# Optimization experiments

Hardware: AMD Instinct MI355X
Metric: run time of the kernel (lower is better)

Reference implementation:

```python
import jax, jax.numpy as jnp
import numpy as np
from jax import lax

N, CIN, COUT = 4, 3, 16
D = H = W = 64
K, S, PAD, OUT_PAD = 3, 2, 1, 1


def setup_inputs() -> dict:
    key = jax.random.key(0)
    k1, k2, k3, k4 = jax.random.split(key, 4)
    x = jax.random.normal(k1, (N, CIN, D, H, W), dtype=jnp.float32)
    # torch ConvTranspose3d weight layout: [Cin, Cout, kD, kH, kW]
    w = jax.random.normal(k2, (CIN, COUT, K, K, K), dtype=jnp.float32) * 0.1
    b = jax.random.normal(k3, (COUT,), dtype=jnp.float32) * 0.1
    subtract = jax.random.normal(k4, (COUT,), dtype=jnp.float32) * 0.1
    return {"x": x, "w": w, "b": b, "subtract": subtract}


def reference(x, w, b, subtract):
    # ConvTranspose3d(k=3, s=2, p=1, output_padding=1) as a dilated conv:
    # flip kernel spatially, swap in/out channel axes, lhs_dilation = stride,
    # padding low = k-1-p = 1, padding high = k-1-p+output_padding = 2.
    w_conv = jnp.flip(jnp.transpose(w, (1, 0, 2, 3, 4)), axis=(2, 3, 4))  # [Cout,Cin,k,k,k]
    y = lax.conv_general_dilated(
        x, w_conv,
        window_strides=(1, 1, 1),
        padding=[(1, 2), (1, 2), (1, 2)],
        lhs_dilation=(S, S, S),
        dimension_numbers=("NCDHW", "OIDHW", "NCDHW"),
    )  # [N, 16, 2D, 2H, 2W]
    y = y + b[None, :, None, None, None]
    # MaxPool3d(kernel=2, stride=2, pad=0)
    y = lax.reduce_window(
        y, -jnp.inf, lax.max,
        window_dimensions=(1, 1, 2, 2, 2),
        window_strides=(1, 1, 2, 2, 2),
        padding="VALID",
    )  # [N, 16, D, H, W]
    s = jax.nn.softmax(y, axis=1)                       # channel softmax
    z = s - subtract[None, :, None, None, None]          # per-channel subtract
    sw = z * jax.nn.sigmoid(z)                           # swish
    return jnp.max(sw, axis=1)                           # max over channels -> [N, D, H, W]
```

## Files before the change

### kernel.cpp

```cpp
#include <hip/hip_runtime.h>
#include <math.h>

#define CIN 3
#define COUT 16
#define DHW 64


typedef float f8 __attribute__((ext_vector_type(8)));
typedef float f2 __attribute__((ext_vector_type(2)));

struct WBuf { f8 a, b, c; f2 d2; float dl; };

template <int G>
static __device__ __forceinline__ void wload(WBuf& b, const float* wbase) {
    constexpr int CO = G / 3, C = G % 3;
    constexpr int BOFF = (C * COUT + CO) * 27 * 4;
    asm volatile(
        "s_load_dwordx8 %0, %5, %6\n\t"
        "s_load_dwordx8 %1, %5, %7\n\t"
        "s_load_dwordx8 %2, %5, %8\n\t"
        "s_load_dwordx2 %3, %5, %9\n\t"
        "s_load_dword   %4, %5, %10"
        : "=s"(b.a), "=s"(b.b), "=s"(b.c), "=s"(b.d2), "=s"(b.dl)
        : "s"(wbase), "i"(BOFF), "i"(BOFF + 32), "i"(BOFF + 64),
          "i"(BOFF + 96), "i"(BOFF + 104));
}

static __device__ __forceinline__ void wwait(WBuf& b) {
    asm volatile("s_waitcnt lgkmcnt(0)"
                 : "+s"(b.a), "+s"(b.b), "+s"(b.c), "+s"(b.d2), "+s"(b.dl));
}

static __device__ __forceinline__ float welem(const WBuf& w, int k) {
    return k < 8 ? w.a[k] : k < 16 ? w.b[k - 8] : k < 24 ? w.c[k - 16]
                 : k < 26 ? w.d2[k - 24] : w.dl;
}

template <int C>
static __device__ __forceinline__ void fma_group(
    const WBuf& wb, const float (&xr)[CIN][3][2][3], float (&acc)[8][4]) {
#pragma unroll
    for (int kd = 0; kd < 3; ++kd) {
        const int pd  = (kd == 1) ? 0 : 1;
        const int dlt = (kd == 0) ? 1 : 0;
#pragma unroll
        for (int kh = 0; kh < 3; ++kh) {
            const int ph = (kh == 1) ? 0 : 1;
            const int hh = (kh == 0) ? 1 : 0;
#pragma unroll
            for (int kw = 0; kw < 3; ++kw) {
                const int pw = (kw == 1) ? 0 : 1;
                const int ww = (kw == 0) ? 1 : 0;
                const float wt = welem(wb, kd * 9 + kh * 3 + kw);
                const int q = (pd * 2 + ph) * 2 + pw;
#pragma unroll
                for (int dout = 0; dout < 2; ++dout)
#pragma unroll
                    for (int vx = 0; vx < 2; ++vx) {
                        const float xv = xr[C][dout + dlt][hh][ww + vx];
                        const int v = dout * 2 + vx;
                        if (C == 0 && kd < 2 && kh < 2 && kw < 2)
                            acc[q][v] = wt * xv;
                        else
                            acc[q][v] = fmaf(wt, xv, acc[q][v]);
                    }
            }
        }
    }
}

static __device__ __forceinline__ void pool_close(const float (&acc)[8][4],
                                                  float (&pc)[4]) {
#pragma unroll
    for (int v = 0; v < 4; ++v) {
        const float m01 = fmaxf(acc[0][v], acc[1][v]);
        const float m23 = fmaxf(acc[2][v], acc[3][v]);
        const float m45 = fmaxf(acc[4][v], acc[5][v]);
        const float m67 = fmaxf(acc[6][v], acc[7][v]);
        pc[v] = fmaxf(fmaxf(m01, m23), fmaxf(m45, m67));
    }
}

template <int G>
struct Pipe {
    static __device__ __forceinline__ void run(
        WBuf& A, WBuf& B, const float* w, const float (&xr)[CIN][3][2][3],
        float (&acc)[8][4], float (&pooled)[COUT][4]) {
        constexpr int CO = G / 3, C = G % 3;
        WBuf& CUR = (G & 1) ? B : A;
        WBuf& NXT = (G & 1) ? A : B;
        wwait(CUR);
        __builtin_amdgcn_sched_barrier(0);
        if constexpr (G + 1 < CIN * COUT) wload<G + 1>(NXT, w);
        fma_group<C>(CUR, xr, acc);
        if constexpr (C == 2) pool_close(acc, pooled[CO]);
        Pipe<G + 1>::run(A, B, w, xr, acc, pooled);
    }
};
template <>
struct Pipe<CIN * COUT> {
    static __device__ __forceinline__ void run(
        WBuf&, WBuf&, const float*, const float (&)[CIN][3][2][3],
        float (&)[8][4], float (&)[COUT][4]) {}
};

__global__ __launch_bounds__(256)
__attribute__((amdgpu_waves_per_eu(2, 2)))
void fused_convt_pool_softmax_swish_max(
    const float* __restrict__ x,
    const float* __restrict__ w,
    const float* __restrict__ bias,
    const float* __restrict__ sub,
    float* __restrict__ out)
{
    const int tp = threadIdx.x;
    const int h  = blockIdx.x * blockDim.y + threadIdx.y;
    const int d0 = blockIdx.y * 2;
    const int n  = blockIdx.z;
    const int w0 = tp * 2;

    float xr[CIN][3][2][3];
    const size_t nbase = (size_t)n * CIN * DHW * DHW * DHW;
    const bool w2ok = (w0 + 2 < DHW);
    const int  off2 = w2ok ? 2 : 0;
#pragma unroll
    for (int c = 0; c < CIN; ++c)
#pragma unroll
        for (int dd = 0; dd < 3; ++dd)
#pragma unroll
            for (int hh = 0; hh < 2; ++hh) {
                const int id = d0 + dd;
                const int ih = h + hh;
                float v0 = 0.0f, v1 = 0.0f, v2 = 0.0f;
                if (id < DHW && ih < DHW) {
                    const float* row =
                        x + nbase + (((size_t)c * DHW + id) * DHW + ih) * DHW + w0;
                    const float2 a = *(const float2*)row;
                    v0 = a.x;
                    v1 = a.y;
                    const float t = row[off2];
                    v2 = w2ok ? t : 0.0f;
                }
                xr[c][dd][hh][0] = v0;
                xr[c][dd][hh][1] = v1;
                xr[c][dd][hh][2] = v2;
            }

    float pooled[COUT][4];
    float acc[8][4];
    WBuf A, B;
    wload<0>(A, w);
    Pipe<0>::run(A, B, w, xr, acc, pooled);

#pragma unroll
    for (int dout = 0; dout < 2; ++dout) {
        float res[2];
#pragma unroll
        for (int vx = 0; vx < 2; ++vx) {
            const int v = dout * 2 + vx;
            float pv[COUT];
#pragma unroll
            for (int co = 0; co < COUT; ++co) pv[co] = pooled[co][v] + bias[co];
            float m = pv[0];
#pragma unroll
            for (int co = 1; co < COUT; ++co) m = fmaxf(m, pv[co]);
            float e[COUT];
            float s = 0.0f;
#pragma unroll
            for (int co = 0; co < COUT; ++co) {
                const float ev = __expf(pv[co] - m);
                e[co] = ev;
                s += ev;
            }
            const float inv = __builtin_amdgcn_rcpf(s);
            float zmax = -3.402823466e+38f;
#pragma unroll
            for (int co = 0; co < COUT; ++co)
                zmax = fmaxf(zmax, fmaf(e[co], inv, -sub[co]));
            res[vx] = zmax * __builtin_amdgcn_rcpf(1.0f + __expf(-zmax));
        }
        float2 r2; r2.x = res[0]; r2.y = res[1];
        float* op = out + (((size_t)n * DHW + (d0 + dout)) * DHW + h) * DHW + w0;
        *(float2*)op = r2;
    }
}

extern "C" void kernel_launch(void* const* d_in, const int* in_sizes, int n_in,
                              void* d_out, int out_size, void* d_ws, size_t ws_size,
                              hipStream_t stream) {
    const float* x   = (const float*)d_in[0];
    const float* w   = (const float*)d_in[1];
    const float* b   = (const float*)d_in[2];
    const float* sub = (const float*)d_in[3];
    float* out = (float*)d_out;

    dim3 block(32, 8, 1);
    dim3 grid(DHW / 8, DHW / 2, 4);
    fused_convt_pool_softmax_swish_max<<<grid, block, 0, stream>>>(x, w, b, sub, out);
}
```

Before: 114.1 us.

## Split output channels across waves and exchange pooled values through LDS

Each of the four waves in a block now computes 4 of the 16 output channels for the same 2x64 spatial tile, instead of one wave computing all 16 channels for its own tile. This gives four times as many blocks and cuts per-thread FMA work and register pressure, and the waves_per_eu cap is removed to allow more occupancy. The pooled, biased values go into a shared-memory buffer. After a barrier, each thread runs the channel softmax, subtract, swish and max for one voxel. The cost is that each input tile is loaded four times, plus an LDS round trip and a block-wide sync, and the output stores become scalar rather than float2.

```diff
diff --git a/kernel.cpp b/kernel.cpp
--- a/kernel.cpp
+++ b/kernel.cpp
@@ -12,16 +12,16 @@
 struct WBuf { f8 a, b, c; f2 d2; float dl; };
 
 template <int G>
-static __device__ __forceinline__ void wload(WBuf& b, const float* wbase) {
-    constexpr int CO = G / 3, C = G % 3;
-    constexpr int BOFF = (C * COUT + CO) * 27 * 4;
+static __device__ __forceinline__ void wload(WBuf& b, const char* wbase) {
+    constexpr int J = G / 3, C = G % 3;
+    constexpr int BOFF = (C * COUT + J) * 27 * 4;
     asm volatile(
         "s_load_dwordx8 %0, %5, %6\n\t"
         "s_load_dwordx8 %1, %5, %7\n\t"
         "s_load_dwordx8 %2, %5, %8\n\t"
         "s_load_dwordx2 %3, %5, %9\n\t"
         "s_load_dword   %4, %5, %10"
-        : "=s"(b.a), "=s"(b.b), "=s"(b.c), "=s"(b.d2), "=s"(b.dl)
+        : "=&s"(b.a), "=&s"(b.b), "=&s"(b.c), "=&s"(b.d2), "=&s"(b.dl)
         : "s"(wbase), "i"(BOFF), "i"(BOFF + 32), "i"(BOFF + 64),
           "i"(BOFF + 96), "i"(BOFF + 104));
 }
@@ -84,40 +84,45 @@
 template <int G>
 struct Pipe {
     static __device__ __forceinline__ void run(
-        WBuf& A, WBuf& B, const float* w, const float (&xr)[CIN][3][2][3],
-        float (&acc)[8][4], float (&pooled)[COUT][4]) {
-        constexpr int CO = G / 3, C = G % 3;
+        WBuf& A, WBuf& B, const char* wbase, const float (&xr)[CIN][3][2][3],
+        float (&acc)[8][4], float (&pooled)[4][4]) {
+        constexpr int J = G / 3, C = G % 3;
         WBuf& CUR = (G & 1) ? B : A;
         WBuf& NXT = (G & 1) ? A : B;
         wwait(CUR);
         __builtin_amdgcn_sched_barrier(0);
-        if constexpr (G + 1 < CIN * COUT) wload<G + 1>(NXT, w);
+        if constexpr (G + 1 < 4 * CIN) wload<G + 1>(NXT, wbase);
         fma_group<C>(CUR, xr, acc);
-        if constexpr (C == 2) pool_close(acc, pooled[CO]);
-        Pipe<G + 1>::run(A, B, w, xr, acc, pooled);
+        if constexpr (C == 2) pool_close(acc, pooled[J]);
+        Pipe<G + 1>::run(A, B, wbase, xr, acc, pooled);
     }
 };
 template <>
-struct Pipe<CIN * COUT> {
+struct Pipe<4 * CIN> {
     static __device__ __forceinline__ void run(
-        WBuf&, WBuf&, const float*, const float (&)[CIN][3][2][3],
-        float (&)[8][4], float (&)[COUT][4]) {}
+        WBuf&, WBuf&, const char*, const float (&)[CIN][3][2][3],
+        float (&)[8][4], float (&)[4][4]) {}
 };
 
-__global__ __launch_bounds__(256)
-__attribute__((amdgpu_waves_per_eu(2, 2)))
-void fused_convt_pool_softmax_swish_max(
+__global__ __launch_bounds__(256) void fused_convt_pool_softmax_swish_max(
     const float* __restrict__ x,
     const float* __restrict__ w,
     const float* __restrict__ bias,
     const float* __restrict__ sub,
     float* __restrict__ out)
 {
-    const int tp = threadIdx.x;
-    const int h  = blockIdx.x * blockDim.y + threadIdx.y;
-    const int d0 = blockIdx.y * 2;
-    const int n  = blockIdx.z;
-    const int w0 = tp * 2;
+    __shared__ float xch[COUT][256];
+
+    const int tid  = threadIdx.x;
+    const int lane = tid & 63;
+    const int wv   = __builtin_amdgcn_readfirstlane(tid >> 6);
+    const int tp   = lane & 31;
+    const int hr   = lane >> 5;
+    const int hb   = blockIdx.x * 2;
+    const int d0   = blockIdx.y * 2;
+    const int n    = blockIdx.z;
+    const int h    = hb + hr;
+    const int w0   = tp * 2;
 
     float xr[CIN][3][2][3];
     const size_t nbase = (size_t)n * CIN * DHW * DHW * DHW;
@@ -145,44 +150,58 @@
                 xr[c][dd][hh][1] = v1;
                 xr[c][dd][hh][2] = v2;
             }
-
-    float pooled[COUT][4];
+#pragma unroll
+    for (int i = 0; i < CIN * 3 * 2 * 3; ++i)
+        asm volatile("" : "+v"(((float*)xr)[i]));
+
+    const char* wbase = (const char*)w + (size_t)wv * 4 * 27 * 4;
+    float pooled[4][4];
     float acc[8][4];
     WBuf A, B;
-    wload<0>(A, w);
-    Pipe<0>::run(A, B, w, xr, acc, pooled);
-
-#pragma unroll
-    for (int dout = 0; dout < 2; ++dout) {
-        float res[2];
-#pragma unroll
-        for (int vx = 0; vx < 2; ++vx) {
-            const int v = dout * 2 + vx;
-            float pv[COUT];
-#pragma unroll
-            for (int co = 0; co < COUT; ++co) pv[co] = pooled[co][v] + bias[co];
-            float m = pv[0];
-#pragma unroll
-            for (int co = 1; co < COUT; ++co) m = fmaxf(m, pv[co]);
-            float e[COUT];
-            float s = 0.0f;
-#pragma unroll
-            for (int co = 0; co < COUT; ++co) {
-                const float ev = __expf(pv[co] - m);
-                e[co] = ev;
-                s += ev;
-            }
-            const float inv = __builtin_amdgcn_rcpf(s);
-            float zmax = -3.402823466e+38f;
-#pragma unroll
-            for (int co = 0; co < COUT; ++co)
-                zmax = fmaxf(zmax, fmaf(e[co], inv, -sub[co]));
-            res[vx] = zmax * __builtin_amdgcn_rcpf(1.0f + __expf(-zmax));
-        }
-        float2 r2; r2.x = res[0]; r2.y = res[1];
-        float* op = out + (((size_t)n * DHW + (d0 + dout)) * DHW + h) * DHW + w0;
-        *(float2*)op = r2;
-    }
+    wload<0>(A, wbase);
+    Pipe<0>::run(A, B, wbase, xr, acc, pooled);
+
+    const float* bj = (const float*)((const char*)bias + (size_t)wv * 16);
+#pragma unroll
+    for (int j = 0; j < 4; ++j) {
+        const float b = bj[j];
+        float4 v;
+        v.x = pooled[j][0] + b;
+        v.y = pooled[j][1] + b;
+        v.z = pooled[j][2] + b;
+        v.w = pooled[j][3] + b;
+        *(float4*)&xch[wv * 4 + j][lane * 4] = v;
+    }
+    __syncthreads();
+
+    float pv[COUT];
+#pragma unroll
+    for (int co = 0; co < COUT; ++co) pv[co] = xch[co][tid];
+    float m = pv[0];
+#pragma unroll
+    for (int co = 1; co < COUT; ++co) m = fmaxf(m, pv[co]);
+    float e[COUT];
+    float s = 0.0f;
+#pragma unroll
+    for (int co = 0; co < COUT; ++co) {
+        const float ev = __expf(pv[co] - m);
+        e[co] = ev;
+        s += ev;
+    }
+    const float inv = __builtin_amdgcn_rcpf(s);
+    float zmax = -3.402823466e+38f;
+#pragma unroll
+    for (int co = 0; co < COUT; ++co)
+        zmax = fmaxf(zmax, fmaf(e[co], inv, -sub[co]));
+    const float res = zmax * __builtin_amdgcn_rcpf(1.0f + __expf(-zmax));
+
+    const int vox  = tid & 3;
+    const int sl   = tid >> 2;
+    const int dout = vox >> 1;
+    const int vx   = vox & 1;
+    const int stp  = sl & 31;
+    const int shr  = sl >> 5;
+    out[(((size_t)n * DHW + (d0 + dout)) * DHW + (hb + shr)) * DHW + stp * 2 + vx] = res;
 }
 
 extern "C" void kernel_launch(void* const* d_in, const int* in_sizes, int n_in,
@@ -194,7 +213,7 @@
     const float* sub = (const float*)d_in[3];
     float* out = (float*)d_out;
 
-    dim3 block(32, 8, 1);
-    dim3 grid(DHW / 8, DHW / 2, 4);
+    dim3 block(256, 1, 1);
+    dim3 grid(DHW / 2, DHW / 2, 4);
     fused_convt_pool_softmax_swish_max<<<grid, block, 0, stream>>>(x, w, b, sub, out);
 }
```

Result: slower. 118.0 us (+3.4%).

## Compute one output depth per thread with smaller blocks to cut register pressure

Applied to the files above, without the earlier changes.

Each thread now produces 2 outputs (one depth slice) instead of 4 (two depth slices), so the input register tile shrinks from 3 to 2 depth rows and the accumulator and pooled arrays halve. Blocks shrink to 128 threads, the grid doubles in depth, and the forced waves-per-EU attribute is dropped so occupancy can rise. The trade-off is that every thread reloads the full weight set through scalar loads and one input depth row is shared less, which raises weight-load and input traffic per output.

```diff
diff --git a/kernel.cpp b/kernel.cpp
--- a/kernel.cpp
+++ b/kernel.cpp
@@ -12,7 +12,7 @@
 struct WBuf { f8 a, b, c; f2 d2; float dl; };
 
 template <int G>
-static __device__ __forceinline__ void wload(WBuf& b, const float* wbase) {
+static __device__ __forceinline__ void wload(WBuf& b, const char* wbase) {
     constexpr int CO = G / 3, C = G % 3;
     constexpr int BOFF = (C * COUT + CO) * 27 * 4;
     asm volatile(
@@ -21,7 +21,7 @@
         "s_load_dwordx8 %2, %5, %8\n\t"
         "s_load_dwordx2 %3, %5, %9\n\t"
         "s_load_dword   %4, %5, %10"
-        : "=s"(b.a), "=s"(b.b), "=s"(b.c), "=s"(b.d2), "=s"(b.dl)
+        : "=&s"(b.a), "=&s"(b.b), "=&s"(b.c), "=&s"(b.d2), "=&s"(b.dl)
         : "s"(wbase), "i"(BOFF), "i"(BOFF + 32), "i"(BOFF + 64),
           "i"(BOFF + 96), "i"(BOFF + 104));
 }
@@ -38,11 +38,11 @@
 
 template <int C>
 static __device__ __forceinline__ void fma_group(
-    const WBuf& wb, const float (&xr)[CIN][3][2][3], float (&acc)[8][4]) {
+    const WBuf& wb, const float (&xr)[CIN][2][2][3], float (&acc)[8][2]) {
 #pragma unroll
     for (int kd = 0; kd < 3; ++kd) {
-        const int pd  = (kd == 1) ? 0 : 1;
-        const int dlt = (kd == 0) ? 1 : 0;
+        const int pd = (kd == 1) ? 0 : 1;
+        const int dd = (kd == 0) ? 1 : 0;
 #pragma unroll
         for (int kh = 0; kh < 3; ++kh) {
             const int ph = (kh == 1) ? 0 : 1;
@@ -54,59 +54,54 @@
                 const float wt = welem(wb, kd * 9 + kh * 3 + kw);
                 const int q = (pd * 2 + ph) * 2 + pw;
 #pragma unroll
-                for (int dout = 0; dout < 2; ++dout)
-#pragma unroll
-                    for (int vx = 0; vx < 2; ++vx) {
-                        const float xv = xr[C][dout + dlt][hh][ww + vx];
-                        const int v = dout * 2 + vx;
-                        if (C == 0 && kd < 2 && kh < 2 && kw < 2)
-                            acc[q][v] = wt * xv;
-                        else
-                            acc[q][v] = fmaf(wt, xv, acc[q][v]);
-                    }
+                for (int vx = 0; vx < 2; ++vx) {
+                    const float xv = xr[C][dd][hh][ww + vx];
+                    if (C == 0 && kd < 2 && kh < 2 && kw < 2)
+                        acc[q][vx] = wt * xv;
+                    else
+                        acc[q][vx] = fmaf(wt, xv, acc[q][vx]);
+                }
             }
         }
     }
 }
 
-static __device__ __forceinline__ void pool_close(const float (&acc)[8][4],
-                                                  float (&pc)[4]) {
+static __device__ __forceinline__ void pool_close(const float (&acc)[8][2],
+                                                  float (&pc)[2]) {
 #pragma unroll
-    for (int v = 0; v < 4; ++v) {
-        const float m01 = fmaxf(acc[0][v], acc[1][v]);
-        const float m23 = fmaxf(acc[2][v], acc[3][v]);
-        const float m45 = fmaxf(acc[4][v], acc[5][v]);
-        const float m67 = fmaxf(acc[6][v], acc[7][v]);
-        pc[v] = fmaxf(fmaxf(m01, m23), fmaxf(m45, m67));
+    for (int vx = 0; vx < 2; ++vx) {
+        const float m01 = fmaxf(acc[0][vx], acc[1][vx]);
+        const float m23 = fmaxf(acc[2][vx], acc[3][vx]);
+        const float m45 = fmaxf(acc[4][vx], acc[5][vx]);
+        const float m67 = fmaxf(acc[6][vx], acc[7][vx]);
+        pc[vx] = fmaxf(fmaxf(m01, m23), fmaxf(m45, m67));
     }
 }
 
 template <int G>
 struct Pipe {
     static __device__ __forceinline__ void run(
-        WBuf& A, WBuf& B, const float* w, const float (&xr)[CIN][3][2][3],
-        float (&acc)[8][4], float (&pooled)[COUT][4]) {
+        WBuf& A, WBuf& B, const char* wbase, const float (&xr)[CIN][2][2][3],
+        float (&acc)[8][2], float (&pooled)[COUT][2]) {
         constexpr int CO = G / 3, C = G % 3;
         WBuf& CUR = (G & 1) ? B : A;
         WBuf& NXT = (G & 1) ? A : B;
         wwait(CUR);
         __builtin_amdgcn_sched_barrier(0);
-        if constexpr (G + 1 < CIN * COUT) wload<G + 1>(NXT, w);
+        if constexpr (G + 1 < CIN * COUT) wload<G + 1>(NXT, wbase);
         fma_group<C>(CUR, xr, acc);
         if constexpr (C == 2) pool_close(acc, pooled[CO]);
-        Pipe<G + 1>::run(A, B, w, xr, acc, pooled);
+        Pipe<G + 1>::run(A, B, wbase, xr, acc, pooled);
     }
 };
 template <>
 struct Pipe<CIN * COUT> {
     static __device__ __forceinline__ void run(
-        WBuf&, WBuf&, const float*, const float (&)[CIN][3][2][3],
-        float (&)[8][4], float (&)[COUT][4]) {}
+        WBuf&, WBuf&, const char*, const float (&)[CIN][2][2][3],
+        float (&)[8][2], float (&)[COUT][2]) {}
 };
 
-__global__ __launch_bounds__(256)
-__attribute__((amdgpu_waves_per_eu(2, 2)))
-void fused_convt_pool_softmax_swish_max(
+__global__ __launch_bounds__(128) void fused_convt_pool_softmax_swish_max(
     const float* __restrict__ x,
     const float* __restrict__ w,
     const float* __restrict__ bias,
@@ -114,22 +109,22 @@
     float* __restrict__ out)
 {
     const int tp = threadIdx.x;
-    const int h  = blockIdx.x * blockDim.y + threadIdx.y;
-    const int d0 = blockIdx.y * 2;
+    const int h  = blockIdx.x * 4 + threadIdx.y;
+    const int d  = blockIdx.y;
     const int n  = blockIdx.z;
     const int w0 = tp * 2;
 
-    float xr[CIN][3][2][3];
+    float xr[CIN][2][2][3];
     const size_t nbase = (size_t)n * CIN * DHW * DHW * DHW;
     const bool w2ok = (w0 + 2 < DHW);
     const int  off2 = w2ok ? 2 : 0;
 #pragma unroll
     for (int c = 0; c < CIN; ++c)
 #pragma unroll
-        for (int dd = 0; dd < 3; ++dd)
+        for (int dd = 0; dd < 2; ++dd)
 #pragma unroll
             for (int hh = 0; hh < 2; ++hh) {
-                const int id = d0 + dd;
+                const int id = d + dd;
                 const int ih = h + hh;
                 float v0 = 0.0f, v1 = 0.0f, v2 = 0.0f;
                 if (id < DHW && ih < DHW) {
@@ -146,43 +141,39 @@
                 xr[c][dd][hh][2] = v2;
             }
 
-    float pooled[COUT][4];
-    float acc[8][4];
+    float pooled[COUT][2];
+    float acc[8][2];
     WBuf A, B;
-    wload<0>(A, w);
-    Pipe<0>::run(A, B, w, xr, acc, pooled);
+    wload<0>(A, (const char*)w);
+    Pipe<0>::run(A, B, (const char*)w, xr, acc, pooled);
 
+    float res[2];
 #pragma unroll
-    for (int dout = 0; dout < 2; ++dout) {
-        float res[2];
+    for (int vx = 0; vx < 2; ++vx) {
+        float pv[COUT];
 #pragma unroll
-        for (int vx = 0; vx < 2; ++vx) {
-            const int v = dout * 2 + vx;
-            float pv[COUT];
+        for (int co = 0; co < COUT; ++co) pv[co] = pooled[co][vx] + bias[co];
+        float m = pv[0];
 #pragma unroll
-            for (int co = 0; co < COUT; ++co) pv[co] = pooled[co][v] + bias[co];
-            float m = pv[0];
+        for (int co = 1; co < COUT; ++co) m = fmaxf(m, pv[co]);
+        float e[COUT];
+        float s = 0.0f;
 #pragma unroll
-            for (int co = 1; co < COUT; ++co) m = fmaxf(m, pv[co]);
-            float e[COUT];
-            float s = 0.0f;
+        for (int co = 0; co < COUT; ++co) {
+            const float ev = __expf(pv[co] - m);
+            e[co] = ev;
+            s += ev;
+        }
+        const float inv = __builtin_amdgcn_rcpf(s);
+        float zmax = -3.402823466e+38f;
 #pragma unroll
-            for (int co = 0; co < COUT; ++co) {
-                const float ev = __expf(pv[co] - m);
-                e[co] = ev;
-                s += ev;
-            }
-            const float inv = __builtin_amdgcn_rcpf(s);
-            float zmax = -3.402823466e+38f;
-#pragma unroll
-            for (int co = 0; co < COUT; ++co)
-                zmax = fmaxf(zmax, fmaf(e[co], inv, -sub[co]));
-            res[vx] = zmax * __builtin_amdgcn_rcpf(1.0f + __expf(-zmax));
-        }
-        float2 r2; r2.x = res[0]; r2.y = res[1];
-        float* op = out + (((size_t)n * DHW + (d0 + dout)) * DHW + h) * DHW + w0;
-        *(float2*)op = r2;
+        for (int co = 0; co < COUT; ++co)
+            zmax = fmaxf(zmax, fmaf(e[co], inv, -sub[co]));
+        res[vx] = zmax * __builtin_amdgcn_rcpf(1.0f + __expf(-zmax));
     }
+    float2 r2; r2.x = res[0]; r2.y = res[1];
+    float* op = out + (((size_t)n * DHW + d) * DHW + h) * DHW + w0;
+    *(float2*)op = r2;
 }
 
 extern "C" void kernel_launch(void* const* d_in, const int* in_sizes, int n_in,
@@ -194,7 +185,7 @@
     const float* sub = (const float*)d_in[3];
     float* out = (float*)d_out;
 
-    dim3 block(32, 8, 1);
-    dim3 grid(DHW / 8, DHW / 2, 4);
+    dim3 block(32, 4, 1);
+    dim3 grid(DHW / 4, DHW, 4);
     fused_convt_pool_softmax_swish_max<<<grid, block, 0, stream>>>(x, w, b, sub, out);
 }
```

Result: faster. 107.8 us (-5.6%).
